# Kernel tuning notes

Measured on AMD Instinct MI355X. Metric: run time of the kernel, lower is better.

## Reference

```python
import jax, jax.numpy as jnp
import numpy as np

B, C, FULLBIN, T = 4, 2, 1025, 1024
BINS = 1024            # n_fft // 2
BANDS = 4
D = BINS // BANDS      # 256
FF = 2048
FF2, FF4 = FF // 2, FF // 4
CROP = 1024
EPS = 1e-5


def layernorm(x, g, b):
    m = jnp.mean(x, axis=-1, keepdims=True)
    v = jnp.mean(jnp.square(x - m), axis=-1, keepdims=True)
    return (x - m) * jax.lax.rsqrt(v + EPS) * g + b


def dconv(x, w, pad):
    # depthwise Conv1d: x (B, Cc, L), w (Cc, 1, K)
    return jax.lax.conv_general_dilated(
        x, w, window_strides=(1,), padding=[(pad, pad)],
        feature_group_count=x.shape[1],
        dimension_numbers=('NCH', 'OIH', 'NCH'))


def pconv(x, w):
    # pointwise Conv1d: x (B, Ci, L), w (Co, Ci, 1)
    return jnp.einsum('bcl,oc->bol', x, w[:, :, 0])


def reference(src, in_w, ln1_g, ln1_b, glu_w, ln2_g, ln2_b,
              c1L_dw, c1L_pw, c1R_dw, c1R_pw, ln3_g, ln3_b,
              c1M_dw, c1M_pw, ln4_g, ln4_b,
              q_w, q_b, qc_w, qc_b, k_w, k_b, v_w, v_b, o_w, o_b, er,
              ln5_g, ln5_b, c2_w, c3_w, out_w):
    s = src[:, :, :BINS]                                 # (B,C,F,T)
    x = jnp.einsum('bcft,c->btf', s, in_w[0])            # in_project + squeeze -> (B,T,BINS)

    # GLU block
    h = layernorm(x, ln1_g, ln1_b)
    g = h @ glu_w.T                                       # (B,T,2*BINS)
    x = x + g[..., :BINS] * jax.nn.sigmoid(g[..., BINS:])

    # conv feed-forward (note: conv1L applied without transpose, as in original)
    h = layernorm(x, ln2_g, ln2_b)
    hL = jax.nn.relu(pconv(dconv(h, c1L_dw, 5), c1L_pw))                          # (B,FF2,BINS)
    hR = jax.nn.relu(pconv(dconv(jnp.swapaxes(h, 1, 2), c1R_dw, 3), c1R_pw))      # (B,FF4,T)
    hR = jnp.swapaxes(hR, 1, 2)                                                   # (B,T,FF4)
    hR = jnp.pad(hR, ((0, 0), (0, 0), (0, BINS - FF4)))
    h = layernorm(hL + hR, ln3_g, ln3_b)                                          # (B,FF2,BINS)
    h = pconv(dconv(jnp.swapaxes(h, 1, 2), c1M_dw, 3), c1M_pw)                    # (B,BINS,FF2)
    x = x + jnp.swapaxes(h, 1, 2)

    # multiband frame attention (q_conv reused for q,k,v as in original)
    h = layernorm(x, ln4_g, ln4_b)

    def qkv(W, bvec):
        y = h @ W.T + bvec
        y = dconv(jnp.swapaxes(y, 1, 2), qc_w, 3) + qc_b[None, :, None]
        return jnp.swapaxes(y, 1, 2).reshape(B, T, BANDS, D)

    q = qkv(q_w, q_b).transpose(0, 2, 1, 3)              # (B,BANDS,T,D)
    k = qkv(k_w, k_b).transpose(0, 2, 3, 1)              # (B,BANDS,D,T)
    v = qkv(v_w, v_b).transpose(0, 2, 1, 3)              # (B,BANDS,T,D)

    p = jnp.pad(q @ er, ((0, 0), (0, 0), (0, 0), (1, 0)))  # (B,BANDS,T,CROP+1)
    p = jnp.swapaxes(p, 2, 3)[:, :, 1:, :]                 # (B,BANDS,CROP,T)
    qk = (q @ k + p) / jnp.sqrt(jnp.float32(BINS))
    a = jax.nn.softmax(qk, axis=-1)
    o = (a @ v).transpose(0, 2, 1, 3).reshape(B, T, BINS) @ o_w.T + o_b
    x = x + o

    # squared-ReLU MLP
    h = layernorm(x, ln5_g, ln5_b)
    h = jnp.square(jax.nn.relu(h @ c2_w.T)) @ c3_w.T
    x = x + h

    # stack back as extra channel, output head, ReLU1, replicate-pad freq row
    t = jnp.swapaxes(x, 1, 2)[:, None]                   # (B,1,BINS,T)
    s2 = jnp.concatenate([s, t], axis=1)                 # (B,C+1,BINS,T)
    y = jnp.einsum('bcft,oc->boft', s2, out_w)           # (B,2,BINS,T)
    y = jnp.clip(y, 0.0, 6.0) / 6.0
    return jnp.concatenate([y, y[:, :, -1:, :]], axis=2)  # (B,2,FULLBIN,T)


def setup_inputs() -> dict:
    key = jax.random.key(0)
    ks = jax.random.split(key, 20)
    n = lambda i, shape, s=0.02: jax.random.normal(ks[i], shape, jnp.float32) * s
    return {
        'src': jax.random.normal(ks[0], (B, C, FULLBIN, T), jnp.float32),
        'in_w': n(1, (1, C)),
        'ln1_g': jnp.ones((BINS,), jnp.float32), 'ln1_b': jnp.zeros((BINS,), jnp.float32),
        'glu_w': n(2, (2 * BINS, BINS)),
        'ln2_g': jnp.ones((BINS,), jnp.float32), 'ln2_b': jnp.zeros((BINS,), jnp.float32),
        'c1L_dw': n(3, (BINS, 1, 11), 0.1), 'c1L_pw': n(4, (FF2, BINS, 1)),
        'c1R_dw': n(5, (BINS, 1, 7), 0.1), 'c1R_pw': n(6, (FF4, BINS, 1)),
        'ln3_g': jnp.ones((FF2,), jnp.float32), 'ln3_b': jnp.zeros((FF2,), jnp.float32),
        'c1M_dw': n(7, (FF2, 1, 7), 0.1), 'c1M_pw': n(8, (BINS, FF2, 1)),
        'ln4_g': jnp.ones((BINS,), jnp.float32), 'ln4_b': jnp.zeros((BINS,), jnp.float32),
        'q_w': n(9, (BINS, BINS)), 'q_b': jnp.zeros((BINS,), jnp.float32),
        'qc_w': n(10, (BINS, 1, 7), 0.1), 'qc_b': jnp.zeros((BINS,), jnp.float32),
        'k_w': n(11, (BINS, BINS)), 'k_b': jnp.zeros((BINS,), jnp.float32),
        'v_w': n(12, (BINS, BINS)), 'v_b': jnp.zeros((BINS,), jnp.float32),
        'o_w': n(13, (BINS, BINS)), 'o_b': jnp.zeros((BINS,), jnp.float32),
        'er': jax.random.normal(ks[14], (D, CROP), jnp.float32),
        'ln5_g': jnp.ones((BINS,), jnp.float32), 'ln5_b': jnp.zeros((BINS,), jnp.float32),
        'c2_w': n(15, (FF, BINS)), 'c3_w': n(16, (BINS, FF)),
        'out_w': n(17, (2, C + 1)),
    }
```

## Files before the change

kernel.cpp:

```cpp
#include <hip/hip_runtime.h>
#include <math.h>


typedef unsigned short u16;
typedef __attribute__((ext_vector_type(4))) float floatx4;
typedef __attribute__((ext_vector_type(8))) short short8;

#define NB 4
static const long long M1 = 1024LL * 1024LL;

__device__ __forceinline__ float bf2f(u16 h) {
    union { unsigned int u; float f; } v;
    v.u = ((unsigned int)h) << 16;
    return v.f;
}
__device__ __forceinline__ u16 f2bf(float x) {
    union { float f; unsigned int u; } v;
    v.f = x;
    unsigned int r = (v.u + 0x7FFFu + ((v.u >> 16) & 1u)) >> 16;
    return (u16)r;
}

__device__ __forceinline__ void async_cp16(const u16* g, u16* lds) {
    __builtin_amdgcn_global_load_lds(
        (const __attribute__((address_space(1))) unsigned int*)g,
        (__attribute__((address_space(3))) unsigned int*)lds, 16, 0, 0);
}

__device__ __forceinline__ float block_sum(float v) {
    __shared__ float sd[4];
    #pragma unroll
    for (int off = 32; off; off >>= 1) v += __shfl_down(v, off, 64);
    int lane = threadIdx.x & 63, wid = threadIdx.x >> 6;
    __syncthreads();
    if (lane == 0) sd[wid] = v;
    __syncthreads();
    return sd[0] + sd[1] + sd[2] + sd[3];
}

template<int BM, int BN, int ACT, int OUT>
__global__ __launch_bounds__(256)
void gemm_bf(const u16* __restrict__ A, const u16* __restrict__ B,
             void* __restrict__ Cv, int K, int lda, int ldb, int ldc,
             long long sAz, long long sBz, long long sCz,
             const float* __restrict__ bias, float scale)
{
    constexpr int MI = BM / 32;
    constexpr int NJ = BN / 32;

    A += (long long)blockIdx.z * sAz;
    B += (long long)blockIdx.z * sBz;
    const long long zc = (long long)blockIdx.z * sCz;

    __shared__ u16 As[BM * 64];
    __shared__ u16 Bs[BN * 64];

    const int id = blockIdx.x + gridDim.x * blockIdx.y;
    const int bx = (id >> 3) % gridDim.x;
    const int by = (id & 7) + 8 * ((id >> 3) / gridDim.x);
    const int m0 = by * BM;
    const int n0 = bx * BN;

    const int lane = threadIdx.x & 63;
    const int w    = threadIdx.x >> 6;
    const int wm   = (w >> 1) * (BM / 2);
    const int wn   = (w & 1) * (BN / 2);
    const int srow = lane >> 2;
    const int scol = (lane & 3) * 8;

    floatx4 acc[MI][NJ];
    #pragma unroll
    for (int i = 0; i < MI; i++)
        #pragma unroll
        for (int j = 0; j < NJ; j++)
            acc[i][j] = floatx4{0.f, 0.f, 0.f, 0.f};

    for (int k0 = 0; k0 < K; k0 += 64) {
        #pragma unroll
        for (int r = 0; r < BM / 32; r++) {
            const int inst = w * (BM / 32) + r;
            const int rg = inst >> 1, kb = inst & 1;
            async_cp16(A + (long long)(m0 + rg * 16 + srow) * lda + k0 + kb * 32 + scol,
                       &As[(rg * 2 + kb) * 512]);
        }
        #pragma unroll
        for (int r = 0; r < BN / 32; r++) {
            const int inst = w * (BN / 32) + r;
            const int rg = inst >> 1, kb = inst & 1;
            async_cp16(B + (long long)(n0 + rg * 16 + srow) * ldb + k0 + kb * 32 + scol,
                       &Bs[(rg * 2 + kb) * 512]);
        }
        __syncthreads();

        #pragma unroll
        for (int s = 0; s < 2; s++) {
            short8 a[MI], b[NJ];
            const int fr = lane & 15;
            const int q  = lane >> 4;
            const int go = (fr * 4 + q) * 8;
            #pragma unroll
            for (int i = 0; i < MI; i++)
                a[i] = *(const short8*)&As[(((wm >> 4) + i) * 2 + s) * 512 + go];
            #pragma unroll
            for (int j = 0; j < NJ; j++)
                b[j] = *(const short8*)&Bs[(((wn >> 4) + j) * 2 + s) * 512 + go];
            #pragma unroll
            for (int i = 0; i < MI; i++)
                #pragma unroll
                for (int j = 0; j < NJ; j++)
                    acc[i][j] = __builtin_amdgcn_mfma_f32_16x16x32_bf16(
                        a[i], b[j], acc[i][j], 0, 0, 0);
        }
        __syncthreads();
    }

    float* Cf = (float*)Cv;
    u16*  Cb  = (u16*)Cv;
    const int cn    = n0 + wn + (lane & 15);
    const int rbase = m0 + wm + (lane >> 4) * 4;
    float bj[NJ];
    #pragma unroll
    for (int j = 0; j < NJ; j++) bj[j] = bias ? bias[cn + j * 16] : 0.f;

    #pragma unroll
    for (int i = 0; i < MI; i++) {
        #pragma unroll
        for (int r = 0; r < 4; r++) {
            const int m = rbase + i * 16 + r;
            #pragma unroll
            for (int j = 0; j < NJ; j++) {
                const int n = cn + j * 16;
                float v = (acc[i][j][r] + bj[j]) * scale;
                if (ACT == 1) v = fmaxf(v, 0.f);
                else if (ACT == 2) { v = fmaxf(v, 0.f); v = v * v; }
                const long long ci = zc + (long long)m * ldc + n;
                if (OUT == 0)      Cf[ci] = v;
                else if (OUT == 1) Cf[ci] += v;
                else if (OUT == 2) Cb[ci] = f2bf(v);
                else               Cb[ci] = f2bf(bf2f(Cb[ci]) + v);
            }
        }
    }
}

__global__ __launch_bounds__(256)
void glugemm_k(const u16* __restrict__ A, const u16* __restrict__ B1,
               const u16* __restrict__ B2, u16* __restrict__ X)
{
    constexpr int BM = 128, BN = 64, MI = 4, NJ = 2;
    __shared__ u16 As[BM * 64];
    __shared__ u16 B1s[BN * 64];
    __shared__ u16 B2s[BN * 64];

    const int id = blockIdx.x + gridDim.x * blockIdx.y;
    const int bx = (id >> 3) % gridDim.x;
    const int by = (id & 7) + 8 * ((id >> 3) / gridDim.x);
    const int m0 = by * BM;
    const int n0 = bx * BN;

    const int lane = threadIdx.x & 63;
    const int w    = threadIdx.x >> 6;
    const int wm   = (w >> 1) * 64;
    const int wn   = (w & 1) * 32;
    const int srow = lane >> 2;
    const int scol = (lane & 3) * 8;

    floatx4 acc1[MI][NJ], acc2[MI][NJ];
    #pragma unroll
    for (int i = 0; i < MI; i++)
        #pragma unroll
        for (int j = 0; j < NJ; j++) {
            acc1[i][j] = floatx4{0.f, 0.f, 0.f, 0.f};
            acc2[i][j] = floatx4{0.f, 0.f, 0.f, 0.f};
        }

    for (int k0 = 0; k0 < 1024; k0 += 64) {
        #pragma unroll
        for (int r = 0; r < 4; r++) {
            const int inst = w * 4 + r;
            const int rg = inst >> 1, kb = inst & 1;
            async_cp16(A + (long long)(m0 + rg * 16 + srow) * 1024 + k0 + kb * 32 + scol,
                       &As[(rg * 2 + kb) * 512]);
        }
        #pragma unroll
        for (int r = 0; r < 2; r++) {
            const int inst = w * 2 + r;
            const int rg = inst >> 1, kb = inst & 1;
            async_cp16(B1 + (long long)(n0 + rg * 16 + srow) * 1024 + k0 + kb * 32 + scol,
                       &B1s[(rg * 2 + kb) * 512]);
            async_cp16(B2 + (long long)(n0 + rg * 16 + srow) * 1024 + k0 + kb * 32 + scol,
                       &B2s[(rg * 2 + kb) * 512]);
        }
        __syncthreads();

        #pragma unroll
        for (int s = 0; s < 2; s++) {
            short8 a[MI], b1[NJ], b2[NJ];
            const int fr = lane & 15;
            const int q  = lane >> 4;
            const int go = (fr * 4 + q) * 8;
            #pragma unroll
            for (int i = 0; i < MI; i++)
                a[i] = *(const short8*)&As[(((wm >> 4) + i) * 2 + s) * 512 + go];
            #pragma unroll
            for (int j = 0; j < NJ; j++) {
                b1[j] = *(const short8*)&B1s[(((wn >> 4) + j) * 2 + s) * 512 + go];
                b2[j] = *(const short8*)&B2s[(((wn >> 4) + j) * 2 + s) * 512 + go];
            }
            #pragma unroll
            for (int i = 0; i < MI; i++)
                #pragma unroll
                for (int j = 0; j < NJ; j++) {
                    acc1[i][j] = __builtin_amdgcn_mfma_f32_16x16x32_bf16(
                        a[i], b1[j], acc1[i][j], 0, 0, 0);
                    acc2[i][j] = __builtin_amdgcn_mfma_f32_16x16x32_bf16(
                        a[i], b2[j], acc2[i][j], 0, 0, 0);
                }
        }
        __syncthreads();
    }

    const int cn    = n0 + wn + (lane & 15);
    const int rbase = m0 + wm + (lane >> 4) * 4;
    #pragma unroll
    for (int i = 0; i < MI; i++)
        #pragma unroll
        for (int r = 0; r < 4; r++) {
            const int m = rbase + i * 16 + r;
            #pragma unroll
            for (int j = 0; j < NJ; j++) {
                const int n = cn + j * 16;
                float g = acc1[i][j][r] / (1.f + expf(-acc2[i][j][r]));
                u16* xp = &X[(long long)m * 1024 + n];
                *xp = f2bf(bf2f(*xp) + g);
            }
        }
}

__global__ __launch_bounds__(256)
void sgemm_exp_k(const u16* __restrict__ A, const u16* __restrict__ B,
                 u16* __restrict__ S, float* __restrict__ rowsum, float scale)
{
    constexpr int MI = 4, NJ = 4;
    const int i0 = blockIdx.x;
    const int x  = i0 & 7;
    const int j0 = i0 >> 3;
    const int z  = x + 8 * (j0 & 1);
    const int t  = j0 >> 1;
    const int bx = t & 7, by = t >> 3;

    A += (long long)z * 524288;
    B += (long long)z * 524288;
    S += (long long)z * M1;
    rowsum += z << 10;

    __shared__ u16 As[128 * 64];
    __shared__ u16 Bs[128 * 64];

    const int m0 = by * 128;
    const int n0 = bx * 128;

    const int lane = threadIdx.x & 63;
    const int w    = threadIdx.x >> 6;
    const int wm   = (w >> 1) * 64;
    const int wn   = (w & 1) * 64;
    const int srow = lane >> 2;
    const int scol = (lane & 3) * 8;

    floatx4 acc[MI][NJ];
    #pragma unroll
    for (int i = 0; i < MI; i++)
        #pragma unroll
        for (int j = 0; j < NJ; j++)
            acc[i][j] = floatx4{0.f, 0.f, 0.f, 0.f};

    for (int k0 = 0; k0 < 512; k0 += 64) {
        #pragma unroll
        for (int r = 0; r < 4; r++) {
            const int inst = w * 4 + r;
            const int rg = inst >> 1, kb = inst & 1;
            async_cp16(A + (long long)(m0 + rg * 16 + srow) * 512 + k0 + kb * 32 + scol,
                       &As[(rg * 2 + kb) * 512]);
            async_cp16(B + (long long)(n0 + rg * 16 + srow) * 512 + k0 + kb * 32 + scol,
                       &Bs[(rg * 2 + kb) * 512]);
        }
        __syncthreads();
        #pragma unroll
        for (int s = 0; s < 2; s++) {
            short8 a[MI], b[NJ];
            const int fr = lane & 15;
            const int q  = lane >> 4;
            const int go = (fr * 4 + q) * 8;
            #pragma unroll
            for (int i = 0; i < MI; i++)
                a[i] = *(const short8*)&As[(((wm >> 4) + i) * 2 + s) * 512 + go];
            #pragma unroll
            for (int j = 0; j < NJ; j++)
                b[j] = *(const short8*)&Bs[(((wn >> 4) + j) * 2 + s) * 512 + go];
            #pragma unroll
            for (int i = 0; i < MI; i++)
                #pragma unroll
                for (int j = 0; j < NJ; j++)
                    acc[i][j] = __builtin_amdgcn_mfma_f32_16x16x32_bf16(
                        a[i], b[j], acc[i][j], 0, 0, 0);
        }
        __syncthreads();
    }

    const int cn    = n0 + wn + (lane & 15);
    const int rbase = m0 + wm + (lane >> 4) * 4;
    #pragma unroll
    for (int i = 0; i < MI; i++)
        #pragma unroll
        for (int r = 0; r < 4; r++) {
            const int m = rbase + i * 16 + r;
            float part = 0.f;
            #pragma unroll
            for (int j = 0; j < NJ; j++) {
                const int n = cn + j * 16;
                float e = expf(acc[i][j][r] * scale);
                S[(long long)m * 1024 + n] = f2bf(e);
                part += e;
            }
            #pragma unroll
            for (int off = 8; off; off >>= 1) part += __shfl_xor(part, off, 64);
            if ((lane & 15) == 0) atomicAdd(&rowsum[m], part);
        }
}

__global__ __launch_bounds__(256)
void aogemm_k(const u16* __restrict__ Sb, const u16* __restrict__ Vt,
              const float* __restrict__ rowsum, u16* __restrict__ AO)
{
    constexpr int MI = 4, NJ = 2;
    const int i0 = blockIdx.x;
    const int x  = i0 & 7;
    const int j0 = i0 >> 3;
    const int z  = x + 8 * (j0 & 1);
    const int t  = j0 >> 1;
    const int bx = t & 3, by = t >> 2;

    Sb += (long long)z * M1;
    Vt += (long long)z * 262144;
    rowsum += z << 10;
    const long long zc = (long long)(z >> 2) * M1 + (z & 3) * 256;

    __shared__ u16 As[128 * 64];
    __shared__ u16 Bs[64 * 64];

    const int m0 = by * 128;
    const int n0 = bx * 64;

    const int lane = threadIdx.x & 63;
    const int w    = threadIdx.x >> 6;
    const int wm   = (w >> 1) * 64;
    const int wn   = (w & 1) * 32;
    const int srow = lane >> 2;
    const int scol = (lane & 3) * 8;

    floatx4 acc[MI][NJ];
    #pragma unroll
    for (int i = 0; i < MI; i++)
        #pragma unroll
        for (int j = 0; j < NJ; j++)
            acc[i][j] = floatx4{0.f, 0.f, 0.f, 0.f};

    for (int k0 = 0; k0 < 1024; k0 += 64) {
        #pragma unroll
        for (int r = 0; r < 4; r++) {
            const int inst = w * 4 + r;
            const int rg = inst >> 1, kb = inst & 1;
            async_cp16(Sb + (long long)(m0 + rg * 16 + srow) * 1024 + k0 + kb * 32 + scol,
                       &As[(rg * 2 + kb) * 512]);
        }
        #pragma unroll
        for (int r = 0; r < 2; r++) {
            const int inst = w * 2 + r;
            const int rg = inst >> 1, kb = inst & 1;
            async_cp16(Vt + (long long)(n0 + rg * 16 + srow) * 1024 + k0 + kb * 32 + scol,
                       &Bs[(rg * 2 + kb) * 512]);
        }
        __syncthreads();
        #pragma unroll
        for (int s = 0; s < 2; s++) {
            short8 a[MI], b[NJ];
            const int fr = lane & 15;
            const int q  = lane >> 4;
            const int go = (fr * 4 + q) * 8;
            #pragma unroll
            for (int i = 0; i < MI; i++)
                a[i] = *(const short8*)&As[(((wm >> 4) + i) * 2 + s) * 512 + go];
            #pragma unroll
            for (int j = 0; j < NJ; j++)
                b[j] = *(const short8*)&Bs[(((wn >> 4) + j) * 2 + s) * 512 + go];
            #pragma unroll
            for (int i = 0; i < MI; i++)
                #pragma unroll
                for (int j = 0; j < NJ; j++)
                    acc[i][j] = __builtin_amdgcn_mfma_f32_16x16x32_bf16(
                        a[i], b[j], acc[i][j], 0, 0, 0);
        }
        __syncthreads();
    }

    const int cn    = n0 + wn + (lane & 15);
    const int rbase = m0 + wm + (lane >> 4) * 4;
    #pragma unroll
    for (int i = 0; i < MI; i++)
        #pragma unroll
        for (int r = 0; r < 4; r++) {
            const int m = rbase + i * 16 + r;
            const float inv = 1.f / rowsum[m];
            #pragma unroll
            for (int j = 0; j < NJ; j++) {
                const int n = cn + j * 16;
                AO[zc + (long long)m * 1024 + n] = f2bf(acc[i][j][r] * inv);
            }
        }
}

__global__ __launch_bounds__(256)
void ln_bf_k(const u16* __restrict__ in, u16* __restrict__ out,
             const float* __restrict__ g, const float* __restrict__ b)
{
    long long row = blockIdx.x;
    int tid = threadIdx.x;
    ushort4 u = ((const ushort4*)(in + (row << 10)))[tid];
    float x0 = bf2f(u.x), x1 = bf2f(u.y), x2 = bf2f(u.z), x3 = bf2f(u.w);
    float s = x0 + x1 + x2 + x3;
    s = block_sum(s);
    float mean = s * (1.f / 1024.f);
    float dx = x0 - mean, dy = x1 - mean, dz = x2 - mean, dw = x3 - mean;
    float s2 = dx * dx + dy * dy + dz * dz + dw * dw;
    s2 = block_sum(s2);
    float inv = rsqrtf(s2 * (1.f / 1024.f) + 1e-5f);
    float4 gg = ((const float4*)g)[tid];
    float4 bb = ((const float4*)b)[tid];
    ushort4 o;
    o.x = f2bf(dx * inv * gg.x + bb.x);
    o.y = f2bf(dy * inv * gg.y + bb.y);
    o.z = f2bf(dz * inv * gg.z + bb.z);
    o.w = f2bf(dw * inv * gg.w + bb.w);
    ((ushort4*)(out + (row << 10)))[tid] = o;
}

__global__ __launch_bounds__(256)
void inproj_k(const float* __restrict__ src, const float* __restrict__ inw,
              u16* __restrict__ X)
{
    __shared__ float tile[32][33];
    int b = blockIdx.z;
    int f0 = blockIdx.y * 32, t0 = blockIdx.x * 32;
    float w0 = inw[0], w1 = inw[1];
    for (int r = threadIdx.y; r < 32; r += 8) {
        int f = f0 + r, t = t0 + threadIdx.x;
        float s0 = src[(((long long)b * 2 + 0) * 1025 + f) * 1024 + t];
        float s1 = src[(((long long)b * 2 + 1) * 1025 + f) * 1024 + t];
        tile[r][threadIdx.x] = w0 * s0 + w1 * s1;
    }
    __syncthreads();
    for (int r = threadIdx.y; r < 32; r += 8)
        X[((long long)b * 1024 + t0 + r) * 1024 + f0 + threadIdx.x] = f2bf(tile[threadIdx.x][r]);
}

__global__ __launch_bounds__(256)
void dconvF_t_k(const u16* __restrict__ in, u16* __restrict__ out,
                const float* __restrict__ w)
{
    __shared__ float itile[32][44];
    __shared__ float otile[32][33];
    int b = blockIdx.z, t0 = blockIdx.y * 32, f0 = blockIdx.x * 32;
    int tx = threadIdx.x & 31, ty = threadIdx.x >> 5;
    for (int r = ty; r < 32; r += 8)
        for (int c = tx; c < 42; c += 32) {
            int f = f0 - 5 + c;
            itile[r][c] = (f >= 0 && f < 1024)
                ? bf2f(in[((long long)(b * 1024 + t0 + r)) * 1024 + f]) : 0.f;
        }
    __syncthreads();
    for (int r = ty; r < 32; r += 8) {
        const float* wr = w + (t0 + r) * 11;
        float acc = 0.f;
        #pragma unroll
        for (int k = 0; k < 11; k++) acc += itile[r][tx + k] * wr[k];
        otile[tx][r] = acc;
    }
    __syncthreads();
    for (int r = ty; r < 32; r += 8)
        out[((long long)(b * 1024 + f0 + r)) * 1024 + t0 + tx] = f2bf(otile[r][tx]);
}

__global__ __launch_bounds__(256)
void dconvT_bf_k(const u16* __restrict__ in, u16* __restrict__ out,
                 const float* __restrict__ w)
{
    int idx = blockIdx.x * 256 + threadIdx.x;
    int f = idx & 1023;
    int bt = idx >> 10;
    int t = bt & 1023;
    int b = bt >> 10;
    const float* wr = w + f * 7;
    float acc = 0.f;
    #pragma unroll
    for (int k = 0; k < 7; k++) {
        int tt = t + k - 3;
        if (tt >= 0 && tt < 1024)
            acc += bf2f(in[(((long long)b << 10) + tt) * 1024 + f]) * wr[k];
    }
    out[idx] = f2bf(acc);
}

__global__ __launch_bounds__(256)
void vconv_t_k(const u16* __restrict__ T3, u16* __restrict__ out,
               const float* __restrict__ w, const float* __restrict__ bias)
{
    __shared__ float itile[38][32];
    __shared__ float otile[32][33];
    int b = blockIdx.z, t0 = blockIdx.y * 32, f0 = blockIdx.x * 32;
    int tx = threadIdx.x & 31, ty = threadIdx.x >> 5;
    for (int i = threadIdx.x; i < 38 * 32; i += 256) {
        int r = i >> 5, c = i & 31;
        int t = t0 - 3 + r;
        itile[r][c] = (t >= 0 && t < 1024)
            ? bf2f(T3[((long long)(b * 1024 + t)) * 3072 + 2048 + f0 + c]) : 0.f;
    }
    __syncthreads();
    for (int r = ty; r < 32; r += 8) {
        const float* wr = w + (f0 + tx) * 7;
        float acc = bias[f0 + tx];
        #pragma unroll
        for (int k = 0; k < 7; k++) acc += itile[r + k][tx] * wr[k];
        otile[tx][r] = acc;
    }
    __syncthreads();
    for (int r = ty; r < 32; r += 8)
        out[((long long)(b * 1024 + f0 + r)) * 1024 + t0 + tx] = f2bf(otile[r][tx]);
}

__global__ __launch_bounds__(256)
void qkpack_k(const u16* __restrict__ T3, const float* __restrict__ w,
              const float* __restrict__ bias, const u16* __restrict__ ertb,
              u16* __restrict__ Apk, u16* __restrict__ Bpk)
{
    int idx = blockIdx.x * 256 + threadIdx.x;
    int f = idx & 1023;
    int t = (idx >> 10) & 1023;
    int b = idx >> 20;
    int band = f >> 8, d = f & 255, z = (b << 2) | band;
    const float* wr = w + f * 7;
    float bq = bias[f];
    float aq = bq, ak = bq;
    #pragma unroll
    for (int k = 0; k < 7; k++) {
        int tt = t + k - 3;
        if (tt >= 0 && tt < 1024) {
            const u16* row = T3 + ((long long)(b << 10) + tt) * 3072 + f;
            float wk = wr[k];
            aq += bf2f(row[0]) * wk;
            ak += bf2f(row[1024]) * wk;
        }
    }
    long long base = (long long)z * 524288 + t * 512 + d;
    u16 qb = f2bf(aq);
    Apk[base] = qb;
    Apk[base + 256] = ertb[t * 256 + d];
    Bpk[base] = f2bf(ak);
    Bpk[base + 256] = qb;
}

struct CastArgs {
    const float* s[10];
    const float* er; const float* qb; const float* kb; const float* vb;
    u16* ert; float* qkvb;
};
__global__ __launch_bounds__(256)
void castall_k(CastArgs a, u16* __restrict__ dst)
{
    const int sz[10] = {2097152, 1048576, 524288, 1048576, 1048576,
                        1048576, 1048576, 1048576, 2097152, 2097152};
    int seg = blockIdx.y;
    int tid = blockIdx.x * 256 + threadIdx.x;
    if (seg < 10) {
        int n = sz[seg];
        int base = 0;
        for (int i = 0; i < seg; i++) base += sz[i];
        int i4 = tid * 4;
        if (i4 >= n) return;
        float4 v = *(const float4*)(a.s[seg] + i4);
        ushort4 o;
        o.x = f2bf(v.x); o.y = f2bf(v.y); o.z = f2bf(v.z); o.w = f2bf(v.w);
        *(ushort4*)(dst + base + i4) = o;
    } else if (seg == 10) {
        if (tid < 262144) {
            int j = tid >> 8, d = tid & 255;
            a.ert[tid] = f2bf(a.er[d * 1024 + j]);
        }
    } else {
        if (tid < 1024) a.qkvb[tid] = a.qb[tid];
        else if (tid < 2048) a.qkvb[tid] = a.kb[tid - 1024];
        else if (tid < 3072) a.qkvb[tid] = a.vb[tid - 2048];
    }
}

__global__ __launch_bounds__(256)
void out_k(const float* __restrict__ src, const u16* __restrict__ X,
           const float* __restrict__ ow, float* __restrict__ out)
{
    __shared__ float tile[32][33];
    int b = blockIdx.z;
    int f0 = blockIdx.y * 32, t0 = blockIdx.x * 32;
    for (int r = threadIdx.y; r < 32; r += 8)
        tile[r][threadIdx.x] = bf2f(X[((long long)b * 1024 + t0 + r) * 1024 + f0 + threadIdx.x]);
    __syncthreads();
    float w00 = ow[0], w01 = ow[1], w02 = ow[2];
    float w10 = ow[3], w11 = ow[4], w12 = ow[5];
    for (int r = threadIdx.y; r < 32; r += 8) {
        int f = f0 + r, t = t0 + threadIdx.x;
        float s0 = src[(((long long)b * 2 + 0) * 1025 + f) * 1024 + t];
        float s1 = src[(((long long)b * 2 + 1) * 1025 + f) * 1024 + t];
        float xv = tile[threadIdx.x][r];
        float v0 = fminf(fmaxf(w00 * s0 + w01 * s1 + w02 * xv, 0.f), 6.f) * (1.f / 6.f);
        float v1 = fminf(fmaxf(w10 * s0 + w11 * s1 + w12 * xv, 0.f), 6.f) * (1.f / 6.f);
        out[(((long long)b * 2 + 0) * 1025 + f) * 1024 + t] = v0;
        out[(((long long)b * 2 + 1) * 1025 + f) * 1024 + t] = v1;
        if (f == 1023) {
            out[(((long long)b * 2 + 0) * 1025 + 1024) * 1024 + t] = v0;
            out[(((long long)b * 2 + 1) * 1025 + 1024) * 1024 + t] = v1;
        }
    }
}

extern "C" void kernel_launch(void* const* d_in, const int* in_sizes, int n_in,
                              void* d_out, int out_size, void* d_ws, size_t ws_size,
                              hipStream_t stream)
{
    const float* src    = (const float*)d_in[0];
    const float* in_w   = (const float*)d_in[1];
    const float* ln1_g  = (const float*)d_in[2];
    const float* ln1_b  = (const float*)d_in[3];
    const float* glu_w  = (const float*)d_in[4];
    const float* ln2_g  = (const float*)d_in[5];
    const float* ln2_b  = (const float*)d_in[6];
    const float* c1L_dw = (const float*)d_in[7];
    const float* c1L_pw = (const float*)d_in[8];
    const float* c1R_dw = (const float*)d_in[9];
    const float* c1R_pw = (const float*)d_in[10];
    const float* ln3_g  = (const float*)d_in[11];
    const float* ln3_b  = (const float*)d_in[12];
    const float* c1M_dw = (const float*)d_in[13];
    const float* c1M_pw = (const float*)d_in[14];
    const float* ln4_g  = (const float*)d_in[15];
    const float* ln4_b  = (const float*)d_in[16];
    const float* q_w    = (const float*)d_in[17];
    const float* q_b    = (const float*)d_in[18];
    const float* qc_w   = (const float*)d_in[19];
    const float* qc_b   = (const float*)d_in[20];
    const float* k_w    = (const float*)d_in[21];
    const float* k_b    = (const float*)d_in[22];
    const float* v_w    = (const float*)d_in[23];
    const float* v_b    = (const float*)d_in[24];
    const float* o_w    = (const float*)d_in[25];
    const float* o_b    = (const float*)d_in[26];
    const float* er     = (const float*)d_in[27];
    const float* ln5_g  = (const float*)d_in[28];
    const float* ln5_b  = (const float*)d_in[29];
    const float* c2_w   = (const float*)d_in[30];
    const float* c3_w   = (const float*)d_in[31];
    const float* out_w  = (const float*)d_in[32];
    float* out = (float*)d_out;

    const size_t MB = 1ull << 20;
    if (ws_size < 162 * MB) return;
    char* wsb = (char*)d_ws;
    u16* X       = (u16*)(wsb + 0);
    u16* SB      = (u16*)(wsb + 8 * MB);
    u16* Apk     = (u16*)(wsb + 32 * MB);
    u16* Bpk     = (u16*)(wsb + 48 * MB);
    u16* Hbf     = (u16*)(wsb + 64 * MB);
    u16* T1bf    = (u16*)(wsb + 72 * MB);
    u16* T3      = (u16*)(wsb + 72 * MB);
    float* rowsum= (float*)(wsb + 72 * MB);
    u16* AO      = (u16*)(wsb + 80 * MB);
    u16* T2bf    = (u16*)(wsb + 96 * MB);
    u16* Vt      = (u16*)(wsb + 96 * MB);
    u16* Sbf     = (u16*)(wsb + 104 * MB);
    u16* Gbf     = (u16*)(wsb + 104 * MB);
    u16* W0      = (u16*)(wsb + 136 * MB);

    u16* glu_wb  = W0;
    u16* c1L_pwb = W0 + 2097152;
    u16* c1R_pwb = W0 + 3145728;
    u16* c1M_pwb = W0 + 3670016;
    u16* qkv_wb  = W0 + 4718592;
    u16* o_wb    = W0 + 7864320;
    u16* c2_wb   = W0 + 8912896;
    u16* c3_wb   = W0 + 11010048;
    u16* ertb    = W0 + 13107200;
    float* qkvb  = (float*)(W0 + 13369344);

    const dim3 blk256(256);
    const dim3 tgrid(32, 32, NB);
    const dim3 tblk(32, 8);
    const int EW = 16384;

    CastArgs ca;
    ca.s[0] = glu_w;  ca.s[1] = c1L_pw; ca.s[2] = c1R_pw; ca.s[3] = c1M_pw;
    ca.s[4] = q_w;    ca.s[5] = k_w;    ca.s[6] = v_w;    ca.s[7] = o_w;
    ca.s[8] = c2_w;   ca.s[9] = c3_w;
    ca.er = er; ca.qb = q_b; ca.kb = k_b; ca.vb = v_b;
    ca.ert = ertb; ca.qkvb = qkvb;
    castall_k<<<dim3(2048, 12), blk256, 0, stream>>>(ca, W0);

    inproj_k<<<tgrid, tblk, 0, stream>>>(src, in_w, X);
    ln_bf_k<<<4096, blk256, 0, stream>>>(X, Hbf, ln1_g, ln1_b);
    glugemm_k<<<dim3(16, 32, 1), blk256, 0, stream>>>(
        Hbf, glu_wb, glu_wb + 1048576, X);
    ln_bf_k<<<4096, blk256, 0, stream>>>(X, Hbf, ln2_g, ln2_b);
    dconvF_t_k<<<tgrid, blk256, 0, stream>>>(Hbf, T2bf, c1L_dw);
    gemm_bf<128, 64, 1, 2><<<dim3(16, 8, NB), blk256, 0, stream>>>(
        c1L_pwb, T2bf, SB, 1024, 1024, 1024, 1024, 0, M1, M1, nullptr, 1.f);
    dconvT_bf_k<<<EW, blk256, 0, stream>>>(Hbf, T1bf, c1R_dw);
    gemm_bf<128, 64, 1, 3><<<dim3(8, 32, 1), blk256, 0, stream>>>(
        T1bf, c1R_pwb, SB, 1024, 1024, 1024, 1024, 0, 0, 0, nullptr, 1.f);
    ln_bf_k<<<4096, blk256, 0, stream>>>(SB, Hbf, ln3_g, ln3_b);
    dconvT_bf_k<<<EW, blk256, 0, stream>>>(Hbf, T1bf, c1M_dw);
    gemm_bf<128, 64, 0, 3><<<dim3(16, 32, 1), blk256, 0, stream>>>(
        T1bf, c1M_pwb, X, 1024, 1024, 1024, 1024, 0, 0, 0, nullptr, 1.f);
    ln_bf_k<<<4096, blk256, 0, stream>>>(X, Hbf, ln4_g, ln4_b);
    gemm_bf<128, 128, 0, 2><<<dim3(24, 32, 1), blk256, 0, stream>>>(
        Hbf, qkv_wb, T3, 1024, 1024, 1024, 3072, 0, 0, 0, qkvb, 1.f);
    qkpack_k<<<EW, blk256, 0, stream>>>(T3, qc_w, qc_b, ertb, Apk, Bpk);
    vconv_t_k<<<tgrid, blk256, 0, stream>>>(T3, Vt, qc_w, qc_b);
    hipMemsetAsync(rowsum, 0, 16 * 1024 * sizeof(float), stream);
    sgemm_exp_k<<<1024, blk256, 0, stream>>>(Apk, Bpk, Sbf, rowsum, 0.03125f);
    aogemm_k<<<512, blk256, 0, stream>>>(Sbf, Vt, rowsum, AO);
    gemm_bf<128, 64, 0, 3><<<dim3(16, 32, 1), blk256, 0, stream>>>(
        AO, o_wb, X, 1024, 1024, 1024, 1024, 0, 0, 0, o_b, 1.f);
    ln_bf_k<<<4096, blk256, 0, stream>>>(X, Hbf, ln5_g, ln5_b);
    gemm_bf<128, 128, 2, 2><<<dim3(16, 32, 1), blk256, 0, stream>>>(
        Hbf, c2_wb, Gbf, 1024, 1024, 1024, 2048, 0, 0, 0, nullptr, 1.f);
    gemm_bf<128, 64, 0, 3><<<dim3(16, 32, 1), blk256, 0, stream>>>(
        Gbf, c3_wb, X, 2048, 2048, 2048, 1024, 0, 0, 0, nullptr, 1.f);
    out_k<<<tgrid, tblk, 0, stream>>>(src, X, out_w, out);
}
```

Baseline: 587.2 us.

## Merge small launches and read Q/K/Er directly in score GEMM instead of packing

Folds the weight cast with the input projection, the two depthwise convs on the same input, and the Q/K pack with the V conv and the rowsum clear into single launches with block-index dispatch. This removes several kernel launches and a memset. The score GEMM now picks its K-dimension source per 32-column chunk, taking Q, K and the transposed Er straight from separate buffers. That drops the duplicated packed A/B buffers that stored Q twice plus a copy of Er, which cuts write traffic, at the cost of a small branch in the load address computation.

```diff
diff --git a/kernel.cpp b/kernel.cpp
--- a/kernel.cpp
+++ b/kernel.cpp
@@ -238,7 +238,8 @@
 }
 
 __global__ __launch_bounds__(256)
-void sgemm_exp_k(const u16* __restrict__ A, const u16* __restrict__ B,
+void sgemm_exp_k(const u16* __restrict__ Qpk, const u16* __restrict__ Kpk,
+                 const u16* __restrict__ ErT,
                  u16* __restrict__ S, float* __restrict__ rowsum, float scale)
 {
     constexpr int MI = 4, NJ = 4;
@@ -249,8 +250,8 @@
     const int t  = j0 >> 1;
     const int bx = t & 7, by = t >> 3;
 
-    A += (long long)z * 524288;
-    B += (long long)z * 524288;
+    const u16* Aq = Qpk + (long long)z * 262144;
+    const u16* Bk = Kpk + (long long)z * 262144;
     S += (long long)z * M1;
     rowsum += z << 10;
 
@@ -279,10 +280,17 @@
         for (int r = 0; r < 4; r++) {
             const int inst = w * 4 + r;
             const int rg = inst >> 1, kb = inst & 1;
-            async_cp16(A + (long long)(m0 + rg * 16 + srow) * 512 + k0 + kb * 32 + scol,
-                       &As[(rg * 2 + kb) * 512]);
-            async_cp16(B + (long long)(n0 + rg * 16 + srow) * 512 + k0 + kb * 32 + scol,
-                       &Bs[(rg * 2 + kb) * 512]);
+            const int cb = k0 + kb * 32;
+            const int ra = m0 + rg * 16 + srow;
+            const u16* sa = (cb < 256)
+                ? Aq  + (long long)ra * 256 + cb + scol
+                : ErT + (long long)ra * 256 + (cb - 256) + scol;
+            async_cp16(sa, &As[(rg * 2 + kb) * 512]);
+            const int rb = n0 + rg * 16 + srow;
+            const u16* sb = (cb < 256)
+                ? Bk + (long long)rb * 256 + cb + scol
+                : Aq + (long long)rb * 256 + (cb - 256) + scol;
+            async_cp16(sb, &Bs[(rg * 2 + kb) * 512]);
         }
         __syncthreads();
         #pragma unroll
@@ -444,50 +452,105 @@
     ((ushort4*)(out + (row << 10)))[tid] = o;
 }
 
-__global__ __launch_bounds__(256)
-void inproj_k(const float* __restrict__ src, const float* __restrict__ inw,
+struct CastArgs {
+    const float* s[10];
+    const float* er; const float* qb; const float* kb; const float* vb;
+    u16* ert; float* qkvb;
+};
+__global__ __launch_bounds__(256)
+void castin_k(CastArgs a, u16* __restrict__ dst,
+              const float* __restrict__ src, const float* __restrict__ inw,
               u16* __restrict__ X)
 {
-    __shared__ float tile[32][33];
-    int b = blockIdx.z;
-    int f0 = blockIdx.y * 32, t0 = blockIdx.x * 32;
-    float w0 = inw[0], w1 = inw[1];
-    for (int r = threadIdx.y; r < 32; r += 8) {
-        int f = f0 + r, t = t0 + threadIdx.x;
-        float s0 = src[(((long long)b * 2 + 0) * 1025 + f) * 1024 + t];
-        float s1 = src[(((long long)b * 2 + 1) * 1025 + f) * 1024 + t];
-        tile[r][threadIdx.x] = w0 * s0 + w1 * s1;
-    }
-    __syncthreads();
-    for (int r = threadIdx.y; r < 32; r += 8)
-        X[((long long)b * 1024 + t0 + r) * 1024 + f0 + threadIdx.x] = f2bf(tile[threadIdx.x][r]);
-}
-
-__global__ __launch_bounds__(256)
-void dconvF_t_k(const u16* __restrict__ in, u16* __restrict__ out,
-                const float* __restrict__ w)
-{
-    __shared__ float itile[32][44];
-    __shared__ float otile[32][33];
-    int b = blockIdx.z, t0 = blockIdx.y * 32, f0 = blockIdx.x * 32;
-    int tx = threadIdx.x & 31, ty = threadIdx.x >> 5;
-    for (int r = ty; r < 32; r += 8)
-        for (int c = tx; c < 42; c += 32) {
-            int f = f0 - 5 + c;
-            itile[r][c] = (f >= 0 && f < 1024)
-                ? bf2f(in[((long long)(b * 1024 + t0 + r)) * 1024 + f]) : 0.f;
-        }
-    __syncthreads();
-    for (int r = ty; r < 32; r += 8) {
-        const float* wr = w + (t0 + r) * 11;
+    const int bid = blockIdx.x;
+    if (bid < 24576) {
+        const int sz[10] = {2097152, 1048576, 524288, 1048576, 1048576,
+                            1048576, 1048576, 1048576, 2097152, 2097152};
+        int seg = bid >> 11;
+        int tid = (bid & 2047) * 256 + threadIdx.x;
+        if (seg < 10) {
+            int n = sz[seg];
+            int base = 0;
+            for (int i = 0; i < seg; i++) base += sz[i];
+            int i4 = tid * 4;
+            if (i4 >= n) return;
+            float4 v = *(const float4*)(a.s[seg] + i4);
+            ushort4 o;
+            o.x = f2bf(v.x); o.y = f2bf(v.y); o.z = f2bf(v.z); o.w = f2bf(v.w);
+            *(ushort4*)(dst + base + i4) = o;
+        } else if (seg == 10) {
+            if (tid < 262144) {
+                int j = tid >> 8, d = tid & 255;
+                a.ert[tid] = f2bf(a.er[d * 1024 + j]);
+            }
+        } else {
+            if (tid < 1024) a.qkvb[tid] = a.qb[tid];
+            else if (tid < 2048) a.qkvb[tid] = a.kb[tid - 1024];
+            else if (tid < 3072) a.qkvb[tid] = a.vb[tid - 2048];
+        }
+    } else {
+        __shared__ float tile[32][33];
+        int ib = bid - 24576;
+        int f0 = (ib & 31) * 32, t0 = ((ib >> 5) & 31) * 32, b = ib >> 10;
+        int tx = threadIdx.x & 31, ty = threadIdx.x >> 5;
+        float w0 = inw[0], w1 = inw[1];
+        for (int r = ty; r < 32; r += 8) {
+            int f = f0 + r, t = t0 + tx;
+            float s0 = src[(((long long)b * 2 + 0) * 1025 + f) * 1024 + t];
+            float s1 = src[(((long long)b * 2 + 1) * 1025 + f) * 1024 + t];
+            tile[r][tx] = w0 * s0 + w1 * s1;
+        }
+        __syncthreads();
+        for (int r = ty; r < 32; r += 8)
+            X[((long long)b * 1024 + t0 + r) * 1024 + f0 + tx] = f2bf(tile[tx][r]);
+    }
+}
+
+__global__ __launch_bounds__(256)
+void dconvFT_k(const u16* __restrict__ in, u16* __restrict__ outT,
+               const float* __restrict__ wT, u16* __restrict__ outF,
+               const float* __restrict__ wF)
+{
+    const int bid = blockIdx.x;
+    if (bid < 16384) {
+        int idx = bid * 256 + threadIdx.x;
+        int f = idx & 1023;
+        int bt = idx >> 10;
+        int t = bt & 1023;
+        int b = bt >> 10;
+        const float* wr = wT + f * 7;
         float acc = 0.f;
         #pragma unroll
-        for (int k = 0; k < 11; k++) acc += itile[r][tx + k] * wr[k];
-        otile[tx][r] = acc;
-    }
-    __syncthreads();
-    for (int r = ty; r < 32; r += 8)
-        out[((long long)(b * 1024 + f0 + r)) * 1024 + t0 + tx] = f2bf(otile[r][tx]);
+        for (int k = 0; k < 7; k++) {
+            int tt = t + k - 3;
+            if (tt >= 0 && tt < 1024)
+                acc += bf2f(in[(((long long)b << 10) + tt) * 1024 + f]) * wr[k];
+        }
+        outT[idx] = f2bf(acc);
+    } else {
+        __shared__ float itile[32][44];
+        __shared__ float otile[32][33];
+        int ib = bid - 16384;
+        int f0 = (ib & 31) * 32, t0 = ((ib >> 5) & 31) * 32, b = ib >> 10;
+        int tx = threadIdx.x & 31, ty = threadIdx.x >> 5;
+        for (int r = ty; r < 32; r += 8)
+            for (int c = tx; c < 42; c += 32) {
+                int f = f0 - 5 + c;
+                itile[r][c] = (f >= 0 && f < 1024)
+                    ? bf2f(in[((long long)(b * 1024 + t0 + r)) * 1024 + f]) : 0.f;
+            }
+        __syncthreads();
+        for (int r = ty; r < 32; r += 8) {
+            const float* wr = wF + (t0 + r) * 11;
+            float acc = 0.f;
+            #pragma unroll
+            for (int k = 0; k < 11; k++) acc += itile[r][tx + k] * wr[k];
+            otile[tx][r] = acc;
+        }
+        __syncthreads();
+        for (int r = ty; r < 32; r += 8)
+            outF[((long long)(b * 1024 + f0 + r)) * 1024 + t0 + tx] = f2bf(otile[r][tx]);
+    }
 }
 
 __global__ __launch_bounds__(256)
@@ -511,94 +574,60 @@
 }
 
 __global__ __launch_bounds__(256)
-void vconv_t_k(const u16* __restrict__ T3, u16* __restrict__ out,
-               const float* __restrict__ w, const float* __restrict__ bias)
-{
-    __shared__ float itile[38][32];
-    __shared__ float otile[32][33];
-    int b = blockIdx.z, t0 = blockIdx.y * 32, f0 = blockIdx.x * 32;
-    int tx = threadIdx.x & 31, ty = threadIdx.x >> 5;
-    for (int i = threadIdx.x; i < 38 * 32; i += 256) {
-        int r = i >> 5, c = i & 31;
-        int t = t0 - 3 + r;
-        itile[r][c] = (t >= 0 && t < 1024)
-            ? bf2f(T3[((long long)(b * 1024 + t)) * 3072 + 2048 + f0 + c]) : 0.f;
-    }
-    __syncthreads();
-    for (int r = ty; r < 32; r += 8) {
-        const float* wr = w + (f0 + tx) * 7;
-        float acc = bias[f0 + tx];
-        #pragma unroll
-        for (int k = 0; k < 7; k++) acc += itile[r + k][tx] * wr[k];
-        otile[tx][r] = acc;
-    }
-    __syncthreads();
-    for (int r = ty; r < 32; r += 8)
-        out[((long long)(b * 1024 + f0 + r)) * 1024 + t0 + tx] = f2bf(otile[r][tx]);
-}
-
-__global__ __launch_bounds__(256)
-void qkpack_k(const u16* __restrict__ T3, const float* __restrict__ w,
-              const float* __restrict__ bias, const u16* __restrict__ ertb,
-              u16* __restrict__ Apk, u16* __restrict__ Bpk)
-{
-    int idx = blockIdx.x * 256 + threadIdx.x;
-    int f = idx & 1023;
-    int t = (idx >> 10) & 1023;
-    int b = idx >> 20;
-    int band = f >> 8, d = f & 255, z = (b << 2) | band;
-    const float* wr = w + f * 7;
-    float bq = bias[f];
-    float aq = bq, ak = bq;
-    #pragma unroll
-    for (int k = 0; k < 7; k++) {
-        int tt = t + k - 3;
-        if (tt >= 0 && tt < 1024) {
-            const u16* row = T3 + ((long long)(b << 10) + tt) * 3072 + f;
-            float wk = wr[k];
-            aq += bf2f(row[0]) * wk;
-            ak += bf2f(row[1024]) * wk;
-        }
-    }
-    long long base = (long long)z * 524288 + t * 512 + d;
-    u16 qb = f2bf(aq);
-    Apk[base] = qb;
-    Apk[base + 256] = ertb[t * 256 + d];
-    Bpk[base] = f2bf(ak);
-    Bpk[base + 256] = qb;
-}
-
-struct CastArgs {
-    const float* s[10];
-    const float* er; const float* qb; const float* kb; const float* vb;
-    u16* ert; float* qkvb;
-};
-__global__ __launch_bounds__(256)
-void castall_k(CastArgs a, u16* __restrict__ dst)
-{
-    const int sz[10] = {2097152, 1048576, 524288, 1048576, 1048576,
-                        1048576, 1048576, 1048576, 2097152, 2097152};
-    int seg = blockIdx.y;
-    int tid = blockIdx.x * 256 + threadIdx.x;
-    if (seg < 10) {
-        int n = sz[seg];
-        int base = 0;
-        for (int i = 0; i < seg; i++) base += sz[i];
-        int i4 = tid * 4;
-        if (i4 >= n) return;
-        float4 v = *(const float4*)(a.s[seg] + i4);
-        ushort4 o;
-        o.x = f2bf(v.x); o.y = f2bf(v.y); o.z = f2bf(v.z); o.w = f2bf(v.w);
-        *(ushort4*)(dst + base + i4) = o;
-    } else if (seg == 10) {
-        if (tid < 262144) {
-            int j = tid >> 8, d = tid & 255;
-            a.ert[tid] = f2bf(a.er[d * 1024 + j]);
-        }
+void qkvpack_k(const u16* __restrict__ T3, const float* __restrict__ w,
+               const float* __restrict__ bias,
+               u16* __restrict__ Qpk, u16* __restrict__ Kpk,
+               u16* __restrict__ Vt, float* __restrict__ rowsum)
+{
+    const int bid = blockIdx.x;
+    if (bid < 16384) {
+        int idx = bid * 256 + threadIdx.x;
+        int f = idx & 1023;
+        int t = (idx >> 10) & 1023;
+        int b = idx >> 20;
+        int band = f >> 8, d = f & 255, z = (b << 2) | band;
+        const float* wr = w + f * 7;
+        float bq = bias[f];
+        float aq = bq, ak = bq;
+        #pragma unroll
+        for (int k = 0; k < 7; k++) {
+            int tt = t + k - 3;
+            if (tt >= 0 && tt < 1024) {
+                const u16* row = T3 + ((long long)(b << 10) + tt) * 3072 + f;
+                float wk = wr[k];
+                aq += bf2f(row[0]) * wk;
+                ak += bf2f(row[1024]) * wk;
+            }
+        }
+        long long base = (long long)z * 262144 + t * 256 + d;
+        Qpk[base] = f2bf(aq);
+        Kpk[base] = f2bf(ak);
+    } else if (bid < 20480) {
+        __shared__ float itile[38][32];
+        __shared__ float otile[32][33];
+        int vb = bid - 16384;
+        int f0 = (vb & 31) * 32, t0 = ((vb >> 5) & 31) * 32, b = vb >> 10;
+        int tx = threadIdx.x & 31, ty = threadIdx.x >> 5;
+        for (int i = threadIdx.x; i < 38 * 32; i += 256) {
+            int r = i >> 5, c = i & 31;
+            int t = t0 - 3 + r;
+            itile[r][c] = (t >= 0 && t < 1024)
+                ? bf2f(T3[((long long)(b * 1024 + t)) * 3072 + 2048 + f0 + c]) : 0.f;
+        }
+        __syncthreads();
+        for (int r = ty; r < 32; r += 8) {
+            const float* wr = w + (f0 + tx) * 7;
+            float acc = bias[f0 + tx];
+            #pragma unroll
+            for (int k = 0; k < 7; k++) acc += itile[r + k][tx] * wr[k];
+            otile[tx][r] = acc;
+        }
+        __syncthreads();
+        for (int r = ty; r < 32; r += 8)
+            Vt[((long long)(b * 1024 + f0 + r)) * 1024 + t0 + tx] = f2bf(otile[r][tx]);
     } else {
-        if (tid < 1024) a.qkvb[tid] = a.qb[tid];
-        else if (tid < 2048) a.qkvb[tid] = a.kb[tid - 1024];
-        else if (tid < 3072) a.qkvb[tid] = a.vb[tid - 2048];
+        int i = (bid - 20480) * 256 + threadIdx.x;
+        rowsum[i] = 0.f;
     }
 }
 
@@ -674,12 +703,12 @@
     char* wsb = (char*)d_ws;
     u16* X       = (u16*)(wsb + 0);
     u16* SB      = (u16*)(wsb + 8 * MB);
-    u16* Apk     = (u16*)(wsb + 32 * MB);
-    u16* Bpk     = (u16*)(wsb + 48 * MB);
+    float* rowsum= (float*)(wsb + 16 * MB);
+    u16* Qpk     = (u16*)(wsb + 32 * MB);
+    u16* Kpk     = (u16*)(wsb + 40 * MB);
     u16* Hbf     = (u16*)(wsb + 64 * MB);
     u16* T1bf    = (u16*)(wsb + 72 * MB);
     u16* T3      = (u16*)(wsb + 72 * MB);
-    float* rowsum= (float*)(wsb + 72 * MB);
     u16* AO      = (u16*)(wsb + 80 * MB);
     u16* T2bf    = (u16*)(wsb + 96 * MB);
     u16* Vt      = (u16*)(wsb + 96 * MB);
@@ -709,17 +738,15 @@
     ca.s[8] = c2_w;   ca.s[9] = c3_w;
     ca.er = er; ca.qb = q_b; ca.kb = k_b; ca.vb = v_b;
     ca.ert = ertb; ca.qkvb = qkvb;
-    castall_k<<<dim3(2048, 12), blk256, 0, stream>>>(ca, W0);
-
-    inproj_k<<<tgrid, tblk, 0, stream>>>(src, in_w, X);
+    castin_k<<<28672, blk256, 0, stream>>>(ca, W0, src, in_w, X);
+
     ln_bf_k<<<4096, blk256, 0, stream>>>(X, Hbf, ln1_g, ln1_b);
     glugemm_k<<<dim3(16, 32, 1), blk256, 0, stream>>>(
         Hbf, glu_wb, glu_wb + 1048576, X);
     ln_bf_k<<<4096, blk256, 0, stream>>>(X, Hbf, ln2_g, ln2_b);
-    dconvF_t_k<<<tgrid, blk256, 0, stream>>>(Hbf, T2bf, c1L_dw);
+    dconvFT_k<<<20480, blk256, 0, stream>>>(Hbf, T1bf, c1R_dw, T2bf, c1L_dw);
     gemm_bf<128, 64, 1, 2><<<dim3(16, 8, NB), blk256, 0, stream>>>(
         c1L_pwb, T2bf, SB, 1024, 1024, 1024, 1024, 0, M1, M1, nullptr, 1.f);
-    dconvT_bf_k<<<EW, blk256, 0, stream>>>(Hbf, T1bf, c1R_dw);
     gemm_bf<128, 64, 1, 3><<<dim3(8, 32, 1), blk256, 0, stream>>>(
         T1bf, c1R_pwb, SB, 1024, 1024, 1024, 1024, 0, 0, 0, nullptr, 1.f);
     ln_bf_k<<<4096, blk256, 0, stream>>>(SB, Hbf, ln3_g, ln3_b);
@@ -729,10 +756,8 @@
     ln_bf_k<<<4096, blk256, 0, stream>>>(X, Hbf, ln4_g, ln4_b);
     gemm_bf<128, 128, 0, 2><<<dim3(24, 32, 1), blk256, 0, stream>>>(
         Hbf, qkv_wb, T3, 1024, 1024, 1024, 3072, 0, 0, 0, qkvb, 1.f);
-    qkpack_k<<<EW, blk256, 0, stream>>>(T3, qc_w, qc_b, ertb, Apk, Bpk);
-    vconv_t_k<<<tgrid, blk256, 0, stream>>>(T3, Vt, qc_w, qc_b);
-    hipMemsetAsync(rowsum, 0, 16 * 1024 * sizeof(float), stream);
-    sgemm_exp_k<<<1024, blk256, 0, stream>>>(Apk, Bpk, Sbf, rowsum, 0.03125f);
+    qkvpack_k<<<20544, blk256, 0, stream>>>(T3, qc_w, qc_b, Qpk, Kpk, Vt, rowsum);
+    sgemm_exp_k<<<1024, blk256, 0, stream>>>(Qpk, Kpk, ertb, Sbf, rowsum, 0.03125f);
     aogemm_k<<<512, blk256, 0, stream>>>(Sbf, Vt, rowsum, AO);
     gemm_bf<128, 64, 0, 3><<<dim3(16, 32, 1), blk256, 0, stream>>>(
         AO, o_wb, X, 1024, 1024, 1024, 1024, 0, 0, 0, o_b, 1.f);
```

Measured after the change: 570.5 us. 2.8% less time.
